# Kernel tuning notes

Measured on AMD Instinct MI355X. Metric: run time of the kernel, lower is better.

The kernel has to match this reference:

```python
import jax, jax.numpy as jnp
import numpy as np

EPS = 1e-5


def _batchnorm(x, gamma, beta):
    # training-mode batch norm over the node axis, per feature channel
    mean = jnp.mean(x, axis=0)
    var = jnp.var(x, axis=0)  # biased variance, as torch uses for normalization
    return (x - mean) * jax.lax.rsqrt(var + EPS) * gamma + beta


def _gcn_conv(h, W, b, src, dst, norm, n_nodes):
    # h: [N, Fin] -> [N, Fout]; D^{-1/2}(A+I)D^{-1/2} (h W) + b
    h = h @ W                                   # [N, Fout]
    msgs = h[src] * norm[:, None]               # [E+N, Fout] gathered, normalized
    out = jax.ops.segment_sum(msgs, dst, num_segments=n_nodes)
    return out + b


def setup_inputs() -> dict:
    key = jax.random.key(0)
    ks = jax.random.split(key, 8)
    N, F, E, H = 50000, 512, 800000, 256
    inp = {
        "x": jax.random.normal(ks[0], (N, F), jnp.float32),
        "edge_index": jax.random.randint(ks[1], (2, E), 0, N, jnp.int64),
        "gamma1": jnp.ones((F,), jnp.float32),
        "beta1": jnp.zeros((F,), jnp.float32),
        "W1": jax.random.normal(ks[2], (F, H), jnp.float32) * (1.0 / np.sqrt(F)),
        "b1": jnp.zeros((H,), jnp.float32),
        "W2": jax.random.normal(ks[3], (H, H), jnp.float32) * (1.0 / np.sqrt(H)),
        "b2": jnp.zeros((H,), jnp.float32),
        "W3": jax.random.normal(ks[4], (H, H), jnp.float32) * (1.0 / np.sqrt(H)),
        "b3": jnp.zeros((H,), jnp.float32),
        "W4": jax.random.normal(ks[5], (H, H), jnp.float32) * (1.0 / np.sqrt(H)),
        "b4": jnp.zeros((H,), jnp.float32),
        "gamma2": jnp.ones((H,), jnp.float32),
        "beta2": jnp.zeros((H,), jnp.float32),
        "Wd": jax.random.normal(ks[6], (H, 5), jnp.float32) * (1.0 / np.sqrt(H)),
        "bd": jnp.zeros((5,), jnp.float32),
    }
    return inp


def reference(x, edge_index, gamma1, beta1, W1, b1, W2, b2, W3, b3, W4, b4,
              gamma2, beta2, Wd, bd):
    N = x.shape[0]
    loops = jnp.arange(N, dtype=edge_index.dtype)
    src = jnp.concatenate([edge_index[0], loops])
    dst = jnp.concatenate([edge_index[1], loops])
    deg = jax.ops.segment_sum(jnp.ones_like(src, dtype=x.dtype), dst, num_segments=N)
    dinv = jax.lax.rsqrt(deg)                    # deg >= 1 due to self-loops
    norm = dinv[src] * dinv[dst]                 # [E+N]

    h = _batchnorm(x, gamma1, beta1)
    h = _gcn_conv(h, W1, b1, src, dst, norm, N)
    h = _gcn_conv(h, W2, b2, src, dst, norm, N)
    h = _gcn_conv(h, W3, b3, src, dst, norm, N)
    h = _gcn_conv(h, W4, b4, src, dst, norm, N)
    h = _batchnorm(h, gamma2, beta2)
    # Flatten(start_dim=1) is identity on [N, 256]
    return jax.nn.sigmoid(h @ Wd + bd)           # [N, 5]
```

## Files before the change

### kernel.cpp

```cpp
#include <hip/hip_runtime.h>
#include <math.h>

#define BN_EPS 1e-5f

typedef float floatx4 __attribute__((ext_vector_type(4)));
typedef short shortx4 __attribute__((ext_vector_type(4)));
typedef short shortx8 __attribute__((ext_vector_type(8)));
typedef __bf16 bf16x8 __attribute__((ext_vector_type(8)));

__device__ __forceinline__ unsigned short f2b(float f) {
    unsigned int u = __builtin_bit_cast(unsigned int, f);
    u += 0x7fffu + ((u >> 16) & 1u);
    return (unsigned short)(u >> 16);
}
__device__ __forceinline__ float b2f(unsigned short s) {
    unsigned int u = ((unsigned int)s) << 16;
    return __builtin_bit_cast(float, u);
}
__device__ __forceinline__ float b2f_s(short s) { return b2f((unsigned short)s); }

__global__ __launch_bounds__(256)
void k_detect(const unsigned int* __restrict__ ei, int n_check, int* __restrict__ flag) {
    __shared__ int any;
    if (threadIdx.x == 0) any = 0;
    __syncthreads();
    for (int i = threadIdx.x; i < n_check; i += 256) {
        if (ei[2 * i + 1] != 0u) any = 1;
    }
    __syncthreads();
    if (threadIdx.x == 0) *flag = any;
}

__global__ __launch_bounds__(256)
void k_convert(const void* __restrict__ ei_raw, const int* __restrict__ flag,
               int* __restrict__ src, int* __restrict__ dst, int* __restrict__ cnt, int E) {
    int e = blockIdx.x * 256 + threadIdx.x;
    if (e >= E) return;
    int s, d;
    if (*flag) {
        const int* a = (const int*)ei_raw;
        s = a[e]; d = a[E + e];
    } else {
        const long long* a = (const long long*)ei_raw;
        s = (int)a[e]; d = (int)a[E + e];
    }
    src[e] = s;
    dst[e] = d;
    atomicAdd(&cnt[d], 1);
}

__global__ __launch_bounds__(1024)
void k_scan_sum(const int* __restrict__ cnt, int* __restrict__ bsum, int N) {
    __shared__ int s[1024];
    int i = blockIdx.x * 1024 + threadIdx.x;
    s[threadIdx.x] = (i < N) ? cnt[i] : 0;
    __syncthreads();
    for (int off = 512; off > 0; off >>= 1) {
        if (threadIdx.x < off) s[threadIdx.x] += s[threadIdx.x + off];
        __syncthreads();
    }
    if (threadIdx.x == 0) bsum[blockIdx.x] = s[0];
}

__global__ __launch_bounds__(1024)
void k_scan_part(int* __restrict__ bsum, int nb) {
    __shared__ int s[1024];
    int t = threadIdx.x;
    int v = (t < nb) ? bsum[t] : 0;
    s[t] = v;
    __syncthreads();
    for (int off = 1; off < 1024; off <<= 1) {
        int tmp = (t >= off) ? s[t - off] : 0;
        __syncthreads();
        s[t] += tmp;
        __syncthreads();
    }
    if (t < nb) bsum[t] = s[t] - v;
}

__global__ __launch_bounds__(1024)
void k_scan_final(const int* __restrict__ cnt, const int* __restrict__ bsum,
                  int* __restrict__ row_ptr, int* __restrict__ cursor,
                  float* __restrict__ dinv, int N) {
    __shared__ int s[1024];
    int b = blockIdx.x, t = threadIdx.x;
    int i = b * 1024 + t;
    int v = (i < N) ? cnt[i] : 0;
    s[t] = v;
    __syncthreads();
    for (int off = 1; off < 1024; off <<= 1) {
        int tmp = (t >= off) ? s[t - off] : 0;
        __syncthreads();
        s[t] += tmp;
        __syncthreads();
    }
    if (i < N) {
        int excl = bsum[b] + s[t] - v;
        row_ptr[i] = excl;
        cursor[i]  = excl;
        dinv[i] = rsqrtf((float)(v + 1));
        if (i == N - 1) row_ptr[N] = excl + v;
    }
}

__global__ __launch_bounds__(256)
void k_fill(const int* __restrict__ src, const int* __restrict__ dst,
            int* __restrict__ cursor, const float* __restrict__ dinv,
            int2* __restrict__ csr_sw, int E) {
    int e = blockIdx.x * 256 + threadIdx.x;
    if (e >= E) return;
    int s = src[e], d = dst[e];
    int p = atomicAdd(&cursor[d], 1);
    float w = dinv[s] * dinv[d];
    csr_sw[p] = make_int2(s, __builtin_bit_cast(int, w));
}

__global__ __launch_bounds__(256)
void k_bnstats_cast(const float* __restrict__ x, unsigned short* __restrict__ xb,
                    float* __restrict__ sum8, float* __restrict__ sumsq8,
                    int NQ, int F) {
    __shared__ float ls[512], lq[512];
    int t   = threadIdx.x;
    int tid = blockIdx.x * 256 + t;
    int G   = gridDim.x * 256;
    int cq  = tid & ((F >> 2) - 1);
    const floatx4* xv = (const floatx4*)x;
    shortx4* xo = (shortx4*)xb;

    float s0 = 0.f, s1 = 0.f, s2 = 0.f, s3 = 0.f;
    float q0 = 0.f, q1 = 0.f, q2 = 0.f, q3 = 0.f;

    int G4 = G << 2;
    int Qfull = NQ - (NQ % G4);
    int i = tid;
    for (; i < Qfull; i += G4) {
        floatx4 a = __builtin_nontemporal_load(&xv[i]);
        floatx4 b = __builtin_nontemporal_load(&xv[i + G]);
        floatx4 c = __builtin_nontemporal_load(&xv[i + 2 * G]);
        floatx4 d = __builtin_nontemporal_load(&xv[i + 3 * G]);
        shortx4 o;
        o[0] = (short)f2b(a[0]); o[1] = (short)f2b(a[1]);
        o[2] = (short)f2b(a[2]); o[3] = (short)f2b(a[3]);
        xo[i] = o;
        s0 += a[0]; s1 += a[1]; s2 += a[2]; s3 += a[3];
        q0 += a[0] * a[0]; q1 += a[1] * a[1]; q2 += a[2] * a[2]; q3 += a[3] * a[3];
        o[0] = (short)f2b(b[0]); o[1] = (short)f2b(b[1]);
        o[2] = (short)f2b(b[2]); o[3] = (short)f2b(b[3]);
        xo[i + G] = o;
        s0 += b[0]; s1 += b[1]; s2 += b[2]; s3 += b[3];
        q0 += b[0] * b[0]; q1 += b[1] * b[1]; q2 += b[2] * b[2]; q3 += b[3] * b[3];
        o[0] = (short)f2b(c[0]); o[1] = (short)f2b(c[1]);
        o[2] = (short)f2b(c[2]); o[3] = (short)f2b(c[3]);
        xo[i + 2 * G] = o;
        s0 += c[0]; s1 += c[1]; s2 += c[2]; s3 += c[3];
        q0 += c[0] * c[0]; q1 += c[1] * c[1]; q2 += c[2] * c[2]; q3 += c[3] * c[3];
        o[0] = (short)f2b(d[0]); o[1] = (short)f2b(d[1]);
        o[2] = (short)f2b(d[2]); o[3] = (short)f2b(d[3]);
        xo[i + 3 * G] = o;
        s0 += d[0]; s1 += d[1]; s2 += d[2]; s3 += d[3];
        q0 += d[0] * d[0]; q1 += d[1] * d[1]; q2 += d[2] * d[2]; q3 += d[3] * d[3];
    }
    for (; i < NQ; i += G) {
        floatx4 a = __builtin_nontemporal_load(&xv[i]);
        shortx4 o;
        o[0] = (short)f2b(a[0]); o[1] = (short)f2b(a[1]);
        o[2] = (short)f2b(a[2]); o[3] = (short)f2b(a[3]);
        xo[i] = o;
        s0 += a[0]; s1 += a[1]; s2 += a[2]; s3 += a[3];
        q0 += a[0] * a[0]; q1 += a[1] * a[1]; q2 += a[2] * a[2]; q3 += a[3] * a[3];
    }

    for (int c = t; c < F; c += 256) { ls[c] = 0.f; lq[c] = 0.f; }
    __syncthreads();
    atomicAdd(&ls[cq * 4 + 0], s0); atomicAdd(&ls[cq * 4 + 1], s1);
    atomicAdd(&ls[cq * 4 + 2], s2); atomicAdd(&ls[cq * 4 + 3], s3);
    atomicAdd(&lq[cq * 4 + 0], q0); atomicAdd(&lq[cq * 4 + 1], q1);
    atomicAdd(&lq[cq * 4 + 2], q2); atomicAdd(&lq[cq * 4 + 3], q3);
    __syncthreads();
    int rep = (blockIdx.x & 7) * F;
    for (int c = t; c < F; c += 256) {
        atomicAdd(&sum8[rep + c],   ls[c]);
        atomicAdd(&sumsq8[rep + c], lq[c]);
    }
}

__global__ __launch_bounds__(256)
void k_bnstats_b(const unsigned short* __restrict__ x, float* __restrict__ sum,
                 float* __restrict__ sumsq, int N, int Mpad, int H) {
    __shared__ float ls[256], lq[256];
    int t     = threadIdx.x;
    int slice = blockIdx.x & 7;
    int bs    = blockIdx.x >> 3;
    int tid_s = bs * 256 + t;
    int G     = (gridDim.x >> 3) * 256;
    int NG    = N * 4;
    const shortx8* xv = (const shortx8*)x + (size_t)slice * Mpad * 4;
    int fq = tid_s & 3;
    float s[8], q[8];
    #pragma unroll
    for (int j = 0; j < 8; ++j) { s[j] = 0.f; q[j] = 0.f; }

    int G2 = G << 1;
    int Qfull = NG - (NG % G2);
    int i = tid_s;
    for (; i < Qfull; i += G2) {
        shortx8 a = __builtin_nontemporal_load(&xv[i]);
        shortx8 b = __builtin_nontemporal_load(&xv[i + G]);
        #pragma unroll
        for (int j = 0; j < 8; ++j) {
            float fa = b2f_s(a[j]);
            float fb = b2f_s(b[j]);
            s[j] += fa + fb;
            q[j] += fa * fa + fb * fb;
        }
    }
    for (; i < NG; i += G) {
        shortx8 a = __builtin_nontemporal_load(&xv[i]);
        #pragma unroll
        for (int j = 0; j < 8; ++j) {
            float fa = b2f_s(a[j]);
            s[j] += fa; q[j] += fa * fa;
        }
    }

    ls[t] = 0.f; lq[t] = 0.f;
    __syncthreads();
    int fg = slice * 4 + fq;
    #pragma unroll
    for (int j = 0; j < 8; ++j) {
        atomicAdd(&ls[fg * 8 + j], s[j]);
        atomicAdd(&lq[fg * 8 + j], q[j]);
    }
    __syncthreads();
    int rep = (bs & 3) * H;
    if ((t >> 5) == slice) {
        atomicAdd(&sum[rep + t],   ls[t]);
        atomicAdd(&sumsq[rep + t], lq[t]);
    }
}

__global__ __launch_bounds__(256)
void k_bnfin(const float* __restrict__ sum, const float* __restrict__ sumsq,
             const float* __restrict__ gamma, const float* __restrict__ beta,
             float* __restrict__ a, float* __restrict__ b, int N, int F, int nrep) {
    int c = blockIdx.x * 256 + threadIdx.x;
    if (c >= F) return;
    float s = 0.f, ss = 0.f;
    for (int i = 0; i < nrep; ++i) { s += sum[i * F + c]; ss += sumsq[i * F + c]; }
    float m   = s / (float)N;
    float var = ss / (float)N - m * m;
    float rs  = rsqrtf(var + BN_EPS);
    float aa  = gamma[c] * rs;
    a[c] = aa;
    b[c] = beta[c] - m * aa;
}

__global__ __launch_bounds__(256)
void k_castWT4(const float* __restrict__ W1, const float* __restrict__ W2,
               const float* __restrict__ W3, const float* __restrict__ W4,
               unsigned short* __restrict__ T1, unsigned short* __restrict__ T2,
               unsigned short* __restrict__ T3, unsigned short* __restrict__ T4,
               const float* __restrict__ bna, int F, int H) {
    int i = blockIdx.x * 256 + threadIdx.x;
    int n1 = F * H, n2 = H * H;
    if (i < n1) {
        int n = i / F, k = i % F;
        T1[i] = f2b(W1[(size_t)k * H + n] * bna[k]);
        return;
    }
    const float* W; unsigned short* T; int j;
    if (i < n1 + n2)          { W = W2; T = T2; j = i - n1; }
    else if (i < n1 + 2 * n2) { W = W3; T = T3; j = i - n1 - n2; }
    else if (i < n1 + 3 * n2) { W = W4; T = T4; j = i - n1 - 2 * n2; }
    else return;
    int n = j / H, k = j % H;
    T[j] = f2b(W[(size_t)k * H + n]);
}

__global__ __launch_bounds__(256)
void k_cvec(const float* __restrict__ W1, const float* __restrict__ bnb,
            float* __restrict__ cvec, int F, int H) {
    int j = threadIdx.x;
    int kslice = F / 8;
    int k0 = blockIdx.x * kslice;
    float s = 0.f;
    for (int k = k0; k < k0 + kslice; ++k)
        s += bnb[k] * W1[(size_t)k * H + j];
    atomicAdd(&cvec[j], s);
}

__device__ __forceinline__ void glds16(const void* g, void* l) {
    __builtin_amdgcn_global_load_lds(
        (const __attribute__((address_space(1))) unsigned int*)g,
        (__attribute__((address_space(3))) unsigned int*)l, 16, 0, 0);
}

__global__ __launch_bounds__(256)
void k_gemm_bf16(const unsigned short* __restrict__ A, const unsigned short* __restrict__ Bt,
                 unsigned short* __restrict__ C, int K, int NC,
                 size_t arow, size_t aks, size_t Mslice) {
    __shared__ unsigned short As[128 * 32];
    __shared__ unsigned short Bs[128 * 32];
    int tid  = threadIdx.x;
    int wave = tid >> 6, lane = tid & 63;
    int row0 = blockIdx.x * 128;
    int col0 = blockIdx.y * 128;
    int wr = (wave & 1) * 64;
    int wc = (wave >> 1) * 64;

    floatx4 acc[4][4];
    #pragma unroll
    for (int i = 0; i < 4; i++)
        #pragma unroll
        for (int j = 0; j < 4; j++) acc[i][j] = (floatx4){0.f, 0.f, 0.f, 0.f};

    int cA = tid * 16;
    int cB = cA + 4096;
    const char* Ab = (const char*)A;
    const char* Bb = (const char*)Bt;
    size_t a_off0 = (size_t)(row0 + (cA >> 6)) * arow + (cA & 63);
    size_t a_off1 = (size_t)(row0 + (cB >> 6)) * arow + (cA & 63);
    size_t b_off0 = (size_t)(col0 + (cA >> 6)) * K * 2 + (cA & 63);
    size_t b_off1 = (size_t)(col0 + (cB >> 6)) * K * 2 + (cA & 63);

    int lm  = lane & 15;
    int lk8 = (lane >> 4) * 8;

    for (int ks = 0; ks < K; ks += 32) {
        size_t abase = (size_t)ks * aks;
        size_t koff  = (size_t)ks * 2;
        glds16(Ab + a_off0 + abase, (char*)As + cA);
        glds16(Ab + a_off1 + abase, (char*)As + cA + 4096);
        glds16(Bb + b_off0 + koff, (char*)Bs + cA);
        glds16(Bb + b_off1 + koff, (char*)Bs + cA + 4096);
        __syncthreads();

        bf16x8 af[4], bfr[4];
        #pragma unroll
        for (int i = 0; i < 4; i++) {
            shortx8 s = *(const shortx8*)&As[(wr + i * 16 + lm) * 32 + lk8];
            af[i] = __builtin_bit_cast(bf16x8, s);
        }
        #pragma unroll
        for (int j = 0; j < 4; j++) {
            shortx8 s = *(const shortx8*)&Bs[(wc + j * 16 + lm) * 32 + lk8];
            bfr[j] = __builtin_bit_cast(bf16x8, s);
        }
        #pragma unroll
        for (int i = 0; i < 4; i++)
            #pragma unroll
            for (int j = 0; j < 4; j++)
                acc[i][j] = __builtin_amdgcn_mfma_f32_16x16x32_bf16(af[i], bfr[j], acc[i][j], 0, 0, 0);
        __syncthreads();
    }

    int crow = row0 + wr + (lane >> 4) * 4;
    int ccol0 = col0 + wc + lm;
    #pragma unroll
    for (int j = 0; j < 4; j++) {
        int c = ccol0 + j * 16;
        size_t cb = (size_t)(c >> 5) * Mslice + (c & 31);
        #pragma unroll
        for (int i = 0; i < 4; i++)
            #pragma unroll
            for (int r = 0; r < 4; r++)
                C[cb + (size_t)(crow + i * 16 + r) * 32] = f2b(acc[i][j][r]);
    }
}

__global__ __launch_bounds__(256)
void k_agg(const unsigned short* __restrict__ hin, unsigned short* __restrict__ hout,
           const int* __restrict__ row_ptr, const int2* __restrict__ csr_sw,
           const float* __restrict__ dinv, const float* __restrict__ bias,
           const float* __restrict__ cvec, int N, int Mpad) {
    int slice = blockIdx.x & 7;
    int nb    = blockIdx.x >> 3;
    int tid   = threadIdx.x;
    int node  = nb * 16 + (tid >> 4);
    if (node >= N) return;
    int eg = (tid >> 2) & 3;
    int fl = tid & 3;
    size_t sbase = (size_t)slice * Mpad * 32;
    const unsigned short* hs = hin + sbase;

    float acc[8];
    float ws = 0.f;
    #pragma unroll
    for (int j = 0; j < 8; ++j) acc[j] = 0.f;
    float di = dinv[node];
    if (eg == 0) {
        shortx8 hv = *(const shortx8*)&hs[(size_t)node * 32 + fl * 8];
        float sl = di * di;
        ws = sl;
        #pragma unroll
        for (int j = 0; j < 8; ++j) acc[j] = b2f_s(hv[j]) * sl;
    }

    int e0 = row_ptr[node], e1 = row_ptr[node + 1];
    const long long* cs = (const long long*)csr_sw;
    for (int e = e0; e < e1; e += 8) {
        int ia = e + eg;
        int ib = e + 4 + eg;
        bool va = ia < e1;
        bool vb = ib < e1;
        long long pa = __builtin_nontemporal_load(&cs[va ? ia : e0]);
        long long pb = __builtin_nontemporal_load(&cs[vb ? ib : e0]);
        int sa = (int)pa, sb = (int)pb;
        float wa = va ? __builtin_bit_cast(float, (int)(pa >> 32)) : 0.f;
        float wb = vb ? __builtin_bit_cast(float, (int)(pb >> 32)) : 0.f;
        shortx8 ra = *(const shortx8*)&hs[(size_t)sa * 32 + fl * 8];
        shortx8 rb = *(const shortx8*)&hs[(size_t)sb * 32 + fl * 8];
        ws += wa + wb;
        #pragma unroll
        for (int j = 0; j < 8; ++j)
            acc[j] += wa * b2f_s(ra[j]) + wb * b2f_s(rb[j]);
    }

    #pragma unroll
    for (int j = 0; j < 8; ++j) {
        acc[j] += __shfl_xor(acc[j], 4, 64);
        acc[j] += __shfl_xor(acc[j], 8, 64);
    }
    ws += __shfl_xor(ws, 4, 64);
    ws += __shfl_xor(ws, 8, 64);

    if (eg == 0) {
        int g = slice * 32 + fl * 8;
        float4 bi0 = *(const float4*)&bias[g];
        float4 bi1 = *(const float4*)&bias[g + 4];
        if (cvec) {
            float4 c0 = *(const float4*)&cvec[g];
            float4 c1 = *(const float4*)&cvec[g + 4];
            bi0.x += ws * c0.x; bi0.y += ws * c0.y;
            bi0.z += ws * c0.z; bi0.w += ws * c0.w;
            bi1.x += ws * c1.x; bi1.y += ws * c1.y;
            bi1.z += ws * c1.z; bi1.w += ws * c1.w;
        }
        shortx8 o;
        o[0] = (short)f2b(acc[0] + bi0.x);
        o[1] = (short)f2b(acc[1] + bi0.y);
        o[2] = (short)f2b(acc[2] + bi0.z);
        o[3] = (short)f2b(acc[3] + bi0.w);
        o[4] = (short)f2b(acc[4] + bi1.x);
        o[5] = (short)f2b(acc[5] + bi1.y);
        o[6] = (short)f2b(acc[6] + bi1.z);
        o[7] = (short)f2b(acc[7] + bi1.w);
        __builtin_nontemporal_store(o, (shortx8*)&hout[sbase + (size_t)node * 32 + fl * 8]);
    }
}

__global__ __launch_bounds__(256)
void k_head(const unsigned short* __restrict__ h, const float* __restrict__ a,
            const float* __restrict__ b, const float* __restrict__ Wd,
            const float* __restrict__ bd, float* __restrict__ out, int N, int Mpad) {
    int node = blockIdx.x * 4 + (threadIdx.x >> 6);
    if (node >= N) return;
    int lane = threadIdx.x & 63;
    int f = lane * 4;
    int slice = lane >> 3;
    int off = (lane & 7) * 4;
    shortx4 hv = *(const shortx4*)&h[(size_t)slice * Mpad * 32 + (size_t)node * 32 + off];
    float v0 = b2f_s(hv[0]) * a[f + 0] + b[f + 0];
    float v1 = b2f_s(hv[1]) * a[f + 1] + b[f + 1];
    float v2 = b2f_s(hv[2]) * a[f + 2] + b[f + 2];
    float v3 = b2f_s(hv[3]) * a[f + 3] + b[f + 3];
    float s[5];
    #pragma unroll
    for (int j = 0; j < 5; ++j) {
        s[j] = v0 * Wd[(f + 0) * 5 + j] + v1 * Wd[(f + 1) * 5 + j] +
               v2 * Wd[(f + 2) * 5 + j] + v3 * Wd[(f + 3) * 5 + j];
    }
    #pragma unroll
    for (int off2 = 32; off2 > 0; off2 >>= 1) {
        #pragma unroll
        for (int j = 0; j < 5; ++j) s[j] += __shfl_down(s[j], off2, 64);
    }
    if (lane == 0) {
        #pragma unroll
        for (int j = 0; j < 5; ++j) {
            float z = s[j] + bd[j];
            out[(size_t)node * 5 + j] = 1.f / (1.f + expf(-z));
        }
    }
}

extern "C" void kernel_launch(void* const* d_in, const int* in_sizes, int n_in,
                              void* d_out, int out_size, void* d_ws, size_t ws_size,
                              hipStream_t stream) {
    const float* x      = (const float*)d_in[0];
    const void*  ei_raw = d_in[1];
    const float* gamma1 = (const float*)d_in[2];
    const float* beta1  = (const float*)d_in[3];
    const float* W1 = (const float*)d_in[4];
    const float* b1 = (const float*)d_in[5];
    const float* W2 = (const float*)d_in[6];
    const float* b2 = (const float*)d_in[7];
    const float* W3 = (const float*)d_in[8];
    const float* b3 = (const float*)d_in[9];
    const float* W4 = (const float*)d_in[10];
    const float* b4 = (const float*)d_in[11];
    const float* gamma2 = (const float*)d_in[12];
    const float* beta2  = (const float*)d_in[13];
    const float* Wd = (const float*)d_in[14];
    const float* bd = (const float*)d_in[15];

    const int F = in_sizes[2];
    const int N = in_sizes[0] / F;
    const int E = in_sizes[1] / 2;
    const int H = in_sizes[5];
    const int Mpad = ((N + 127) / 128) * 128;
    const int NB   = (N + 1023) / 1024;
    const size_t Mslice = (size_t)Mpad * 32;
    float* out = (float*)d_out;

    char* p = (char*)d_ws;
    auto alloc = [&](size_t bytes) {
        void* r = (void*)p;
        p += (bytes + 255) & ~(size_t)255;
        return r;
    };
    int*   flag    = (int*)  alloc(4);
    int*   srcA    = (int*)  alloc((size_t)E * 4);
    int*   dstA    = (int*)  alloc((size_t)E * 4);
    char*  zstart  = p;
    int*   cnt     = (int*)  alloc((size_t)N * 4);
    float* colsum8 = (float*)alloc((size_t)8 * F * 4);
    float* colsq8  = (float*)alloc((size_t)8 * F * 4);
    float* colsum2 = (float*)alloc((size_t)4 * H * 4);
    float* colsq2  = (float*)alloc((size_t)4 * H * 4);
    float* cvec    = (float*)alloc((size_t)H * 4);
    size_t zbytes  = (size_t)(p - zstart);
    int*   row_ptr = (int*)  alloc(((size_t)N + 1) * 4);
    int*   cursor  = (int*)  alloc((size_t)N * 4);
    float* dinv    = (float*)alloc((size_t)N * 4);
    int2*  csr_sw  = (int2*) alloc((size_t)E * 8);
    int*   bsum    = (int*)  alloc((size_t)NB * 4);
    float* bna     = (float*)alloc((size_t)F * 4);
    float* bnb     = (float*)alloc((size_t)F * 4);
    unsigned short* W1t = (unsigned short*)alloc((size_t)F * H * 2);
    unsigned short* W2t = (unsigned short*)alloc((size_t)H * H * 2);
    unsigned short* W3t = (unsigned short*)alloc((size_t)H * H * 2);
    unsigned short* W4t = (unsigned short*)alloc((size_t)H * H * 2);
    unsigned short* xb  = (unsigned short*)alloc((size_t)Mpad * F * 2);
    unsigned short* hbA = (unsigned short*)alloc((size_t)Mpad * H * 2);
    unsigned short* hbB = (unsigned short*)alloc((size_t)Mpad * H * 2);

    hipMemsetAsync(zstart, 0, zbytes, stream);
    hipMemsetAsync(xb + (size_t)N * F, 0, (size_t)(Mpad - N) * F * 2, stream);

    int n_check = (E >= 2048) ? 2048 : E;
    k_detect<<<1, 256, 0, stream>>>((const unsigned int*)ei_raw, n_check, flag);
    k_convert<<<(E + 255) / 256, 256, 0, stream>>>(ei_raw, flag, srcA, dstA, cnt, E);
    k_scan_sum<<<NB, 1024, 0, stream>>>(cnt, bsum, N);
    k_scan_part<<<1, 1024, 0, stream>>>(bsum, NB);
    k_scan_final<<<NB, 1024, 0, stream>>>(cnt, bsum, row_ptr, cursor, dinv, N);
    k_fill<<<(E + 255) / 256, 256, 0, stream>>>(srcA, dstA, cursor, dinv, csr_sw, E);

    int NQ = N * (F >> 2);
    k_bnstats_cast<<<2048, 256, 0, stream>>>(x, xb, colsum8, colsq8, NQ, F);
    k_bnfin<<<(F + 255) / 256, 256, 0, stream>>>(colsum8, colsq8, gamma1, beta1, bna, bnb, N, F, 8);

    int tot = F * H + 3 * H * H;
    k_castWT4<<<(tot + 255) / 256, 256, 0, stream>>>(W1, W2, W3, W4, W1t, W2t, W3t, W4t, bna, F, H);
    k_cvec<<<8, 256, 0, stream>>>(W1, bnb, cvec, F, H);

    dim3 gg(Mpad / 128, H / 128);
    int aggb = ((N + 15) / 16) * 8;
    size_t arow_rm = (size_t)F * 2;
    size_t arow_sm = 64;
    size_t aks_sm  = (size_t)Mpad * 2;
    k_gemm_bf16<<<gg, 256, 0, stream>>>(xb, W1t, hbA, F, H, arow_rm, 2, Mslice);
    k_agg<<<aggb, 256, 0, stream>>>(hbA, hbB, row_ptr, csr_sw, dinv, b1, cvec, N, Mpad);
    k_gemm_bf16<<<gg, 256, 0, stream>>>(hbB, W2t, hbA, H, H, arow_sm, aks_sm, Mslice);
    k_agg<<<aggb, 256, 0, stream>>>(hbA, hbB, row_ptr, csr_sw, dinv, b2, nullptr, N, Mpad);
    k_gemm_bf16<<<gg, 256, 0, stream>>>(hbB, W3t, hbA, H, H, arow_sm, aks_sm, Mslice);
    k_agg<<<aggb, 256, 0, stream>>>(hbA, hbB, row_ptr, csr_sw, dinv, b3, nullptr, N, Mpad);
    k_gemm_bf16<<<gg, 256, 0, stream>>>(hbB, W4t, hbA, H, H, arow_sm, aks_sm, Mslice);
    k_agg<<<aggb, 256, 0, stream>>>(hbA, hbB, row_ptr, csr_sw, dinv, b4, nullptr, N, Mpad);

    k_bnstats_b<<<1024, 256, 0, stream>>>(hbB, colsum2, colsq2, N, Mpad, H);
    k_bnfin<<<(H + 255) / 256, 256, 0, stream>>>(colsum2, colsq2, gamma2, beta2, bna, bnb, N, H, 4);
    k_head<<<(N + 3) / 4, 256, 0, stream>>>(hbB, bna, bnb, Wd, bd, out, N, Mpad);
}
```

Measured before the change: 836.4 us.

## Stage block's CSR edge pairs in shared memory and unroll gather by four

The aggregation kernel now loads the whole contiguous CSR range for its 16 nodes cooperatively into LDS in chunks of 1024, then each thread reads its (src, weight) pairs from LDS instead of issuing scattered global loads. The inner loop also processes four edges per thread per iteration, giving more outstanding feature gathers. This is meant to make the edge-list read coalesced and raise memory-level parallelism. The cost is added block-wide barriers, 8 KB of LDS per block that may limit occupancy, and threads in a block can no longer exit early.

```diff
diff --git a/kernel.cpp b/kernel.cpp
--- a/kernel.cpp
+++ b/kernel.cpp
@@ -373,47 +373,66 @@
            const int* __restrict__ row_ptr, const int2* __restrict__ csr_sw,
            const float* __restrict__ dinv, const float* __restrict__ bias,
            const float* __restrict__ cvec, int N, int Mpad) {
+    __shared__ long long pairs[1024];
     int slice = blockIdx.x & 7;
     int nb    = blockIdx.x >> 3;
     int tid   = threadIdx.x;
-    int node  = nb * 16 + (tid >> 4);
-    if (node >= N) return;
+    int nfirst = nb * 16;
+    int node  = nfirst + (tid >> 4);
+    int nodec = node < N ? node : N - 1;
     int eg = (tid >> 2) & 3;
     int fl = tid & 3;
     size_t sbase = (size_t)slice * Mpad * 32;
     const unsigned short* hs = hin + sbase;
 
+    int nlast = nfirst + 16; if (nlast > N) nlast = N;
+    int e_lo = row_ptr[nfirst];
+    int e_hi = row_ptr[nlast];
+    int e0 = row_ptr[nodec], e1 = row_ptr[nodec + 1];
+
     float acc[8];
     float ws = 0.f;
     #pragma unroll
     for (int j = 0; j < 8; ++j) acc[j] = 0.f;
-    float di = dinv[node];
+    float di = dinv[nodec];
     if (eg == 0) {
-        shortx8 hv = *(const shortx8*)&hs[(size_t)node * 32 + fl * 8];
+        shortx8 hv = *(const shortx8*)&hs[(size_t)nodec * 32 + fl * 8];
         float sl = di * di;
         ws = sl;
         #pragma unroll
         for (int j = 0; j < 8; ++j) acc[j] = b2f_s(hv[j]) * sl;
     }
 
-    int e0 = row_ptr[node], e1 = row_ptr[node + 1];
     const long long* cs = (const long long*)csr_sw;
-    for (int e = e0; e < e1; e += 8) {
-        int ia = e + eg;
-        int ib = e + 4 + eg;
-        bool va = ia < e1;
-        bool vb = ib < e1;
-        long long pa = __builtin_nontemporal_load(&cs[va ? ia : e0]);
-        long long pb = __builtin_nontemporal_load(&cs[vb ? ib : e0]);
-        int sa = (int)pa, sb = (int)pb;
-        float wa = va ? __builtin_bit_cast(float, (int)(pa >> 32)) : 0.f;
-        float wb = vb ? __builtin_bit_cast(float, (int)(pb >> 32)) : 0.f;
-        shortx8 ra = *(const shortx8*)&hs[(size_t)sa * 32 + fl * 8];
-        shortx8 rb = *(const shortx8*)&hs[(size_t)sb * 32 + fl * 8];
-        ws += wa + wb;
-        #pragma unroll
-        for (int j = 0; j < 8; ++j)
-            acc[j] += wa * b2f_s(ra[j]) + wb * b2f_s(rb[j]);
+    for (int cb = e_lo; cb < e_hi; cb += 1024) {
+        int cnt = e_hi - cb; if (cnt > 1024) cnt = 1024;
+        __syncthreads();
+        for (int i = tid; i < cnt; i += 256)
+            pairs[i] = __builtin_nontemporal_load(&cs[cb + i]);
+        __syncthreads();
+        int lo  = e0 > cb ? e0 : cb;
+        int hi_ = e1 < cb + cnt ? e1 : cb + cnt;
+        for (int e = lo; e < hi_; e += 16) {
+            int i0 = e + eg, i1 = i0 + 4, i2 = i0 + 8, i3 = i0 + 12;
+            bool v0 = i0 < hi_, v1 = i1 < hi_, v2 = i2 < hi_, v3 = i3 < hi_;
+            long long p0 = pairs[(v0 ? i0 : lo) - cb];
+            long long p1 = pairs[(v1 ? i1 : lo) - cb];
+            long long p2 = pairs[(v2 ? i2 : lo) - cb];
+            long long p3 = pairs[(v3 ? i3 : lo) - cb];
+            float w0 = v0 ? __builtin_bit_cast(float, (int)(p0 >> 32)) : 0.f;
+            float w1 = v1 ? __builtin_bit_cast(float, (int)(p1 >> 32)) : 0.f;
+            float w2 = v2 ? __builtin_bit_cast(float, (int)(p2 >> 32)) : 0.f;
+            float w3 = v3 ? __builtin_bit_cast(float, (int)(p3 >> 32)) : 0.f;
+            shortx8 r0 = *(const shortx8*)&hs[(size_t)(int)p0 * 32 + fl * 8];
+            shortx8 r1 = *(const shortx8*)&hs[(size_t)(int)p1 * 32 + fl * 8];
+            shortx8 r2 = *(const shortx8*)&hs[(size_t)(int)p2 * 32 + fl * 8];
+            shortx8 r3 = *(const shortx8*)&hs[(size_t)(int)p3 * 32 + fl * 8];
+            ws += (w0 + w1) + (w2 + w3);
+            #pragma unroll
+            for (int j = 0; j < 8; ++j)
+                acc[j] += w0 * b2f_s(r0[j]) + w1 * b2f_s(r1[j])
+                        + w2 * b2f_s(r2[j]) + w3 * b2f_s(r3[j]);
+        }
     }
 
     #pragma unroll
@@ -424,7 +443,7 @@
     ws += __shfl_xor(ws, 4, 64);
     ws += __shfl_xor(ws, 8, 64);
 
-    if (eg == 0) {
+    if (eg == 0 && node < N) {
         int g = slice * 32 + fl * 8;
         float4 bi0 = *(const float4*)&bias[g];
         float4 bi1 = *(const float4*)&bias[g + 4];
```

After: 762.4 us. -8.8%, faster.
